# Kernel optimization log

Measured on AMD Instinct MI355X. Metric: run time of the kernel, lower is better.

## Reference

```python
import jax, jax.numpy as jnp
import numpy as np

N, E, R = 50000, 400000, 500
X_SIZE = 100
G_SIZE = 100
HID = 64
OUT = 64
HEADS = 2
ALPHA = 0.5
NEG_SLOPE = 0.01  # nn.LeakyReLU default and attention slope
EPS = 1e-12       # F.normalize eps


def _l2norm(x, axis):
    return x / jnp.maximum(jnp.linalg.norm(x, axis=axis, keepdims=True), EPS)


def _xavier(key, shape, gain=1.414):
    fan_in, fan_out = shape[-1], int(np.prod(shape[:-1]))
    std = gain * np.sqrt(2.0 / (fan_in + fan_out))
    return jax.random.normal(key, shape, dtype=jnp.float32) * std


def _att_layer(h, g, row, col, etype, W, b, att, out_size):
    # h: [N, D_h], g: [R, D_g], W: [heads*out, 2*D_h+D_g], att: [1, heads, out]
    n = h.shape[0]
    h_ijk = jnp.concatenate([h[row], h[col], g[etype]], axis=1)      # [E, 2D_h+D_g]
    c_ijk = (h_ijk @ W.T + b).reshape(-1, HEADS, out_size)           # [E, H, O]
    a = jnp.sum(att * c_ijk, axis=2, keepdims=True)                  # [E, H, 1]
    e = jnp.exp(jax.nn.leaky_relu(a, NEG_SLOPE))                     # unnormalized (matches torch exp w/o max-sub)
    denom = jax.ops.segment_sum(e, row, num_segments=n)              # [N, H, 1]
    alpha = e / denom[row]
    # self-edge zeros contribute nothing; segment_sum over num_segments=n is equivalent
    return jax.ops.segment_sum(alpha * c_ijk, col, num_segments=n)   # [N, H, O]


def setup_inputs() -> dict:
    key = jax.random.key(0)
    ks = jax.random.split(key, 20)
    x = jax.random.normal(ks[0], (N, X_SIZE), dtype=jnp.float32)
    g = jax.random.normal(ks[1], (R, G_SIZE), dtype=jnp.float32)
    edge_idx = jax.random.randint(ks[2], (2, E), 0, N)
    edge_type = jax.random.randint(ks[3], (E,), 0, R)
    d1 = 2 * X_SIZE + G_SIZE
    d2 = 2 * HID * HEADS + G_SIZE
    inp = {
        "x": x, "g": g, "edge_idx": edge_idx, "edge_type": edge_type,
        "W1i": _xavier(ks[4], (HEADS * HID, d1)), "b1i": jnp.zeros((HEADS * HID,), jnp.float32),
        "a1i": _xavier(ks[5], (1, HEADS, HID)),
        "W1o": _xavier(ks[6], (HEADS * HID, d1)), "b1o": jnp.zeros((HEADS * HID,), jnp.float32),
        "a1o": _xavier(ks[7], (1, HEADS, HID)),
        "W2i": _xavier(ks[8], (HEADS * OUT, d2)), "b2i": jnp.zeros((HEADS * OUT,), jnp.float32),
        "a2i": _xavier(ks[9], (1, HEADS, OUT)),
        "W2o": _xavier(ks[10], (HEADS * OUT, d2)), "b2o": jnp.zeros((HEADS * OUT,), jnp.float32),
        "a2o": _xavier(ks[11], (1, HEADS, OUT)),
        "We": _xavier(ks[12], (HID, X_SIZE)), "be": jnp.zeros((HID,), jnp.float32),
        "Wr": _xavier(ks[13], (HEADS * HID, G_SIZE)), "br": jnp.zeros((HEADS * HID,), jnp.float32),
    }
    return inp


def reference(x, g, edge_idx, edge_type, W1i, b1i, a1i, W1o, b1o, a1o,
              W2i, b2i, a2i, W2o, b2o, a2o, We, be, Wr, br):
    # x = F.normalize(x, dim=1).detach()
    xn = jax.lax.stop_gradient(_l2norm(x, axis=1))
    row, col = edge_idx[0], edge_idx[1]

    h_in = _att_layer(xn, g, row, col, edge_type, W1i, b1i, a1i, HID)
    h_out = _att_layer(xn, g, col, row, edge_type, W1o, b1o, a1o, HID)
    h = jax.nn.leaky_relu(ALPHA * h_in + (1.0 - ALPHA) * h_out, NEG_SLOPE)
    h = _l2norm(h, axis=2)                                # [N, H, HID]
    h = h.transpose(0, 1, 2).reshape(N, HEADS * HID)      # concat heads

    h_in = _att_layer(h, g, row, col, edge_type, W2i, b2i, a2i, OUT)
    h_out = _att_layer(h, g, col, row, edge_type, W2o, b2o, a2o, OUT)
    h = jax.nn.leaky_relu(ALPHA * h_in + (1.0 - ALPHA) * h_out, NEG_SLOPE)
    h = _l2norm(h, axis=2)                                # [N, H, OUT]

    # EntityLayer: Linear(x)[:, None, :] + h  (requires HID == OUT)
    h_prime = (xn @ We.T + be)[:, None, :] + h            # [N, H, OUT]
    h_prime = h_prime.reshape(N, HEADS * OUT)
    h_prime = _l2norm(h_prime, axis=1)                    # (torch dim=2 bug -> last dim)
    # _merge_heads stores mean but returns input unchanged

    g_prime = g @ Wr.T + br                               # [R, HEADS*HID]
    return h_prime, g_prime
```

## Files before the change

### kernel.cpp

```cpp
#include <hip/hip_runtime.h>

typedef unsigned short u16;
typedef unsigned int u32;
typedef short short8v __attribute__((ext_vector_type(8)));
typedef float float4v __attribute__((ext_vector_type(4)));

#define N_NODES 50000
#define E_EDGES 400000
#define R_REL   500
#define NKEYS   100000
#define SCAN_B  98
#define SEG     ((size_t)N_NODES * 128)

__device__ __forceinline__ float bl(u32 u){ return __uint_as_float(u << 16); }
__device__ __forceinline__ float bh(u32 u){ return __uint_as_float(u & 0xffff0000u); }
__device__ __forceinline__ u16 f2b(float f){
    u32 u = __float_as_uint(f);
    return (u16)((u + 0x7fffu + ((u >> 16) & 1u)) >> 16);
}
__device__ __forceinline__ u32 pk2(float a, float b){ return (u32)f2b(a) | ((u32)f2b(b) << 16); }
__device__ __forceinline__ float lrelu(float x){ return x > 0.f ? x : 0.01f * x; }

__global__ void k_norm_x(const float* __restrict__ x, u16* __restrict__ xnb){
    int wid = threadIdx.x >> 6, l = threadIdx.x & 63;
    int n = blockIdx.x * 4 + wid;
    if (n >= N_NODES) return;
    float v0 = x[(size_t)n * 100 + l];
    float v1 = (l + 64 < 100) ? x[(size_t)n * 100 + 64 + l] : 0.f;
    float ss = v0 * v0 + v1 * v1;
    #pragma unroll
    for (int m = 32; m; m >>= 1) ss += __shfl_xor(ss, m);
    float s = 1.f / fmaxf(sqrtf(ss), 1e-12f);
    xnb[(size_t)n * 128 + l] = f2b(v0 * s);
    xnb[(size_t)n * 128 + 64 + l] = (l + 64 < 100) ? f2b(v1 * s) : (u16)0;
}

__global__ void k_build_wcat(const float* __restrict__ W1i, const float* __restrict__ W1o,
                             const float* __restrict__ W2i, const float* __restrict__ W2o,
                             const float* __restrict__ We,
                             const float* __restrict__ a1i, const float* __restrict__ a1o,
                             const float* __restrict__ a2i, const float* __restrict__ a2o,
                             u16* __restrict__ wc1, u16* __restrict__ wc2,
                             float* __restrict__ attcat){
    int idx = blockIdx.x * blockDim.x + threadIdx.x;
    if (idx < 576 * 128){
        int r = idx >> 7, k = idx & 127;
        float v = 0.f;
        if (r < 512){
            int seg = r >> 7, rr = r & 127;
            const float* W = (seg < 2) ? W1i : W1o;
            int off = (seg & 1) ? 100 : 0;
            if (k < 100) v = W[(size_t)rr * 300 + off + k];
        } else {
            int rr = r - 512;
            if (k < 100) v = We[(size_t)rr * 100 + k];
        }
        wc1[idx] = f2b(v);
    } else if (idx < 576 * 128 + 512 * 128){
        int j = idx - 576 * 128;
        int r = j >> 7, k = j & 127;
        int seg = r >> 7, rr = r & 127;
        const float* W = (seg < 2) ? W2i : W2o;
        int off = (seg & 1) ? 128 : 0;
        wc2[j] = f2b(W[(size_t)rr * 356 + off + k]);
    } else if (idx < 576 * 128 + 512 * 128 + 1024){
        int j = idx - (576 * 128 + 512 * 128);
        int s = j >> 9, cc = j & 511;
        const float* a = s ? ((cc < 256) ? a2i : a2o) : ((cc < 256) ? a1i : a1o);
        attcat[j] = a[cc & 127];
    }
}

__global__ void k_pg(const float* __restrict__ g,
                     const float* __restrict__ W1i, const float* __restrict__ W1o,
                     const float* __restrict__ W2i, const float* __restrict__ W2o,
                     const float* __restrict__ b1i, const float* __restrict__ b1o,
                     const float* __restrict__ b2i, const float* __restrict__ b2o,
                     const float* __restrict__ a1i, const float* __restrict__ a1o,
                     const float* __restrict__ a2i, const float* __restrict__ a2o,
                     const float* __restrict__ Wr, const float* __restrict__ br,
                     float* __restrict__ Pg, float* __restrict__ qg,
                     float* __restrict__ out){
    int bid = blockIdx.x;
    int j = threadIdx.x;
    __shared__ float gs[100];
    __shared__ float red[128];
    if (bid >= 2000){
        int r = bid - 2000;
        if (j < 100) gs[j] = g[(size_t)r * 100 + j];
        __syncthreads();
        float acc = br[j];
        #pragma unroll 4
        for (int k = 0; k < 100; ++k) acc += gs[k] * Wr[(size_t)j * 100 + k];
        out[(size_t)N_NODES * 128 + (size_t)r * 128 + j] = acc;
        return;
    }
    int r = bid >> 2, t = bid & 3;
    const float *W, *b, *att; int ld, off;
    if (t == 0){ W = W1i; ld = 300; off = 200; b = b1i; att = a1i; }
    else if (t == 1){ W = W1o; ld = 300; off = 200; b = b1o; att = a1o; }
    else if (t == 2){ W = W2i; ld = 356; off = 256; b = b2i; att = a2i; }
    else { W = W2o; ld = 356; off = 256; b = b2o; att = a2o; }
    if (j < 100) gs[j] = g[(size_t)r * 100 + j];
    __syncthreads();
    float acc = b[j];
    #pragma unroll 4
    for (int k = 0; k < 100; ++k) acc += gs[k] * W[(size_t)j * ld + off + k];
    Pg[((size_t)t * R_REL + r) * 128 + j] = acc;
    red[j] = att[j] * acc;
    __syncthreads();
    if (j < 2){
        float s = 0.f;
        for (int k = 0; k < 64; ++k) s += red[j * 64 + k];
        qg[((size_t)t * R_REL + r) * 2 + j] = s;
    }
}

__launch_bounds__(256)
__global__ void k_gemm(const u16* __restrict__ A, const u16* __restrict__ W,
                       const float* __restrict__ attcat,
                       u16* __restrict__ NPt, float* __restrict__ q, int M, int NN){
    __shared__ __align__(16) char lds[4 * 16 * 272];
    int l = threadIdx.x & 63, w = threadIdx.x >> 6;
    int rb = blockIdx.x * 64 + w * 16;
    int grp = blockIdx.y;
    int cb = grp * 128;
    int ncols = NN - cb; if (ncols > 128) ncols = 128;
    int tiles = ncols >> 4;
    int rowW = (ncols == 128) ? 128 : 64;
    int pitch = rowW * 2 + 16;
    char* lw = lds + w * 16 * pitch;

    int ar = rb + (l & 15); if (ar >= M) ar = M - 1;
    const u16* Ap = A + (size_t)ar * 128 + (l >> 4) * 8;
    short8v a0 = *(const short8v*)(Ap);
    short8v a1 = *(const short8v*)(Ap + 32);
    short8v a2 = *(const short8v*)(Ap + 64);
    short8v a3 = *(const short8v*)(Ap + 96);
    float qa[4] = {0.f, 0.f, 0.f, 0.f};
    bool doq = (cb < 512);
    int rloc0 = (l >> 4) * 4;
    for (int t = 0; t < tiles; ++t){
        int cc = cb + t * 16 + (l & 15);
        const u16* Wp = W + (size_t)cc * 128 + (l >> 4) * 8;
        short8v b0 = *(const short8v*)(Wp);
        short8v b1 = *(const short8v*)(Wp + 32);
        short8v b2 = *(const short8v*)(Wp + 64);
        short8v b3 = *(const short8v*)(Wp + 96);
        float4v acc = {0.f, 0.f, 0.f, 0.f};
        acc = __builtin_amdgcn_mfma_f32_16x16x32_bf16(a0, b0, acc, 0, 0, 0);
        acc = __builtin_amdgcn_mfma_f32_16x16x32_bf16(a1, b1, acc, 0, 0, 0);
        acc = __builtin_amdgcn_mfma_f32_16x16x32_bf16(a2, b2, acc, 0, 0, 0);
        acc = __builtin_amdgcn_mfma_f32_16x16x32_bf16(a3, b3, acc, 0, 0, 0);
        int lcol = t * 16 + (l & 15);
        #pragma unroll
        for (int r = 0; r < 4; ++r)
            *(u16*)(lw + (size_t)(rloc0 + r) * pitch + lcol * 2) = f2b(acc[r]);
        if (doq){
            float av = attcat[cc];
            #pragma unroll
            for (int r = 0; r < 4; ++r) qa[r] += av * acc[r];
            if ((t & 3) == 3){
                int g = (cb >> 6) + (t >> 2);
                #pragma unroll
                for (int r = 0; r < 4; ++r){
                    float s = qa[r];
                    s += __shfl_xor(s, 1); s += __shfl_xor(s, 2);
                    s += __shfl_xor(s, 4); s += __shfl_xor(s, 8);
                    if ((l & 15) == 0){
                        int rr = rb + rloc0 + r;
                        if (rr < M) q[(size_t)rr * 8 + g] = s;
                    }
                    qa[r] = 0.f;
                }
            }
        }
    }
    __syncthreads();
    u16* gb = (rowW == 128) ? (NPt + (size_t)grp * SEG + (size_t)rb * 128)
                            : (NPt + 4 * SEG + (size_t)rb * 64);
    int chunks = (rowW == 128) ? 4 : 2;
    for (int i = 0; i < chunks; ++i){
        int u = i * 512 + l * 8;
        int rloc = (rowW == 128) ? (u >> 7) : (u >> 6);
        int c    = (rowW == 128) ? (u & 127) : (u & 63);
        if (rb + rloc < M){
            short8v v = *(const short8v*)(lw + (size_t)rloc * pitch + c * 2);
            *(short8v*)(gb + u) = v;
        }
    }
}

__global__ void k_hist(const int* __restrict__ ei, u32* __restrict__ cnt){
    int e = blockIdx.x * blockDim.x + threadIdx.x;
    if (e >= E_EDGES) return;
    atomicAdd(&cnt[ei[E_EDGES + e]], 1u);
    atomicAdd(&cnt[N_NODES + ei[e]], 1u);
}

__launch_bounds__(1024)
__global__ void k_scan1(const u32* __restrict__ cnt, u32* __restrict__ off, u32* __restrict__ bsum){
    __shared__ u32 sh[1024];
    int t = threadIdx.x, b = blockIdx.x, idx = b * 1024 + t;
    u32 v = cnt[idx];
    sh[t] = v; __syncthreads();
    #pragma unroll
    for (int d = 1; d < 1024; d <<= 1){
        u32 add = (t >= d) ? sh[t - d] : 0;
        __syncthreads();
        sh[t] += add;
        __syncthreads();
    }
    off[idx] = sh[t] - v;
    if (t == 1023) bsum[b] = sh[1023];
}

__launch_bounds__(1024)
__global__ void k_scan3(u32* __restrict__ off, const u32* __restrict__ bsum,
                        u32* __restrict__ cur){
    __shared__ u32 baseb;
    if (threadIdx.x == 0){
        u32 run = 0;
        for (int i = 0; i < (int)blockIdx.x; ++i) run += bsum[i];
        baseb = run;
    }
    __syncthreads();
    int idx = blockIdx.x * 1024 + threadIdx.x;
    u32 v = off[idx] + baseb;
    off[idx] = v;
    if (idx < NKEYS) cur[idx] = v;
}

__global__ void k_pos(const int* __restrict__ ei, const int* __restrict__ ety,
                      u32* __restrict__ cur,
                      u32* __restrict__ Pso, u32* __restrict__ Pss){
    int e = blockIdx.x * blockDim.x + threadIdx.x;
    if (e >= E_EDGES) return;
    u32 row = (u32)ei[e], col = (u32)ei[E_EDGES + e];
    u32 etb = (u32)ety[e] << 20;
    u32 pI = atomicAdd(&cur[col], 1u);
    Pso[pI] = row | etb;  Pss[pI] = col;
    u32 pO = atomicAdd(&cur[N_NODES + row], 1u);
    Pso[pO] = col | etb;  Pss[pO] = row;
}

__global__ void k_edgeA(const u32* __restrict__ Pso, const u32* __restrict__ Pss,
                        const float* __restrict__ q,
                        const float* __restrict__ qgI, const float* __restrict__ qgO,
                        float2* __restrict__ ex){
    int p = blockIdx.x * blockDim.x + threadIdx.x;
    if (p >= 2 * E_EDGES) return;
    u32 so = Pso[p], self = Pss[p];
    u32 oth = so & 0xFFFFF, et = so >> 20;
    float2 r;
    if (p < E_EDGES){
        r.x = expf(lrelu(q[(size_t)oth * 8 + 0] + q[(size_t)self * 8 + 2] + qgI[(size_t)et * 2 + 0]));
        r.y = expf(lrelu(q[(size_t)oth * 8 + 1] + q[(size_t)self * 8 + 3] + qgI[(size_t)et * 2 + 1]));
    } else {
        r.x = expf(lrelu(q[(size_t)oth * 8 + 4] + q[(size_t)self * 8 + 6] + qgO[(size_t)et * 2 + 0]));
        r.y = expf(lrelu(q[(size_t)oth * 8 + 5] + q[(size_t)self * 8 + 7] + qgO[(size_t)et * 2 + 1]));
    }
    ex[p] = r;
}

__global__ void k_denom(const u32* __restrict__ off, const u32* __restrict__ Pso,
                        const float* __restrict__ q,
                        const float* __restrict__ qgI, const float* __restrict__ qgO,
                        float* __restrict__ rdI, float* __restrict__ rdO){
    int t = blockIdx.x * blockDim.x + threadIdx.x;
    if (t >= 2 * N_NODES) return;
    if (t < N_NODES){
        int n = t;
        float qn0 = q[(size_t)n * 8 + 0], qn1 = q[(size_t)n * 8 + 1];
        float s0 = 0.f, s1 = 0.f;
        for (u32 p = off[N_NODES + n]; p < off[N_NODES + n + 1]; ++p){
            u32 so = Pso[p]; u32 oth = so & 0xFFFFFu, et = so >> 20;
            float2 qo = *(const float2*)(q + (size_t)oth * 8 + 2);
            float2 gq = *(const float2*)(qgI + (size_t)et * 2);
            s0 += expf(lrelu(qn0 + qo.x + gq.x));
            s1 += expf(lrelu(qn1 + qo.y + gq.y));
        }
        rdI[(size_t)n * 2 + 0] = (s0 > 0.f) ? 1.f / s0 : 0.f;
        rdI[(size_t)n * 2 + 1] = (s1 > 0.f) ? 1.f / s1 : 0.f;
    } else {
        int n = t - N_NODES;
        float qn4 = q[(size_t)n * 8 + 4], qn5 = q[(size_t)n * 8 + 5];
        float s0 = 0.f, s1 = 0.f;
        for (u32 p = off[n]; p < off[n + 1]; ++p){
            u32 so = Pso[p]; u32 oth = so & 0xFFFFFu, et = so >> 20;
            float2 qo = *(const float2*)(q + (size_t)oth * 8 + 6);
            float2 gq = *(const float2*)(qgO + (size_t)et * 2);
            s0 += expf(lrelu(qn4 + qo.x + gq.x));
            s1 += expf(lrelu(qn5 + qo.y + gq.y));
        }
        rdO[(size_t)n * 2 + 0] = (s0 > 0.f) ? 1.f / s0 : 0.f;
        rdO[(size_t)n * 2 + 1] = (s1 > 0.f) ? 1.f / s1 : 0.f;
    }
}

__launch_bounds__(256)
__global__ void k_agg(const u32* __restrict__ off,
                      const u32* __restrict__ Pso,
                      const float2* __restrict__ ex,
                      const u16* __restrict__ NPt,
                      const float* __restrict__ PgI, const float* __restrict__ PgO,
                      const float* __restrict__ rdI, const float* __restrict__ rdO,
                      int final_stage,
                      const u16* __restrict__ NPt1, const float* __restrict__ be,
                      u16* __restrict__ h1b, float* __restrict__ out){
    int wid = threadIdx.x >> 6, l = threadIdx.x & 63;
    int n = blockIdx.x * 4 + wid;
    if (n >= N_NODES) return;
    int h = l >> 5, d0 = l * 2;
    const u16* PaI = NPt;
    const u16* PbI = NPt + SEG;
    const u16* PaO = NPt + 2 * SEG;
    const u16* PbO = NPt + 3 * SEG;
    u32 pbi = *(const u32*)(PbI + (size_t)n * 128 + d0);
    u32 pbo = *(const u32*)(PbO + (size_t)n * 128 + d0);

    float a0 = 0.f, a1 = 0.f, sai = 0.f;
    {
        u32 sBeg = __builtin_amdgcn_readfirstlane(off[n]);
        u32 sEnd = __builtin_amdgcn_readfirstlane(off[n + 1]);
        for (u32 p = sBeg; p < sEnd; p += 8){
            u32 so[8]; float2 e2[8];
            #pragma unroll
            for (int j = 0; j < 8; ++j){
                u32 idx = p + j; if (idx >= sEnd) idx = sEnd - 1;
                so[j] = Pso[idx];
                e2[j] = ex[idx];
            }
            float w0[8], w1[8]; u32 pa[8]; float2 gv[8];
            #pragma unroll
            for (int j = 0; j < 8; ++j){
                u32 oth = so[j] & 0xFFFFFu, et = so[j] >> 20;
                float2 rd2 = *(const float2*)(rdI + (size_t)oth * 2);
                float sc = (p + j < sEnd) ? 1.f : 0.f;
                w0[j] = e2[j].x * rd2.x * sc;
                w1[j] = e2[j].y * rd2.y * sc;
                pa[j] = *(const u32*)(PaI + (size_t)oth * 128 + d0);
                gv[j] = *(const float2*)(PgI + (size_t)et * 128 + d0);
            }
            #pragma unroll
            for (int j = 0; j < 8; ++j){
                float w = h ? w1[j] : w0[j];
                a0 += w * (bl(pa[j]) + gv[j].x);
                a1 += w * (bh(pa[j]) + gv[j].y);
                sai += w;
            }
        }
    }
    a0 += sai * bl(pbi);
    a1 += sai * bh(pbi);

    float b0 = 0.f, b1 = 0.f, sao = 0.f;
    {
        u32 sBeg = __builtin_amdgcn_readfirstlane(off[N_NODES + n]);
        u32 sEnd = __builtin_amdgcn_readfirstlane(off[N_NODES + n + 1]);
        for (u32 p = sBeg; p < sEnd; p += 8){
            u32 so[8]; float2 e2[8];
            #pragma unroll
            for (int j = 0; j < 8; ++j){
                u32 idx = p + j; if (idx >= sEnd) idx = sEnd - 1;
                so[j] = Pso[idx];
                e2[j] = ex[idx];
            }
            float w0[8], w1[8]; u32 pa[8]; float2 gv[8];
            #pragma unroll
            for (int j = 0; j < 8; ++j){
                u32 oth = so[j] & 0xFFFFFu, et = so[j] >> 20;
                float2 rd2 = *(const float2*)(rdO + (size_t)oth * 2);
                float sc = (p + j < sEnd) ? 1.f : 0.f;
                w0[j] = e2[j].x * rd2.x * sc;
                w1[j] = e2[j].y * rd2.y * sc;
                pa[j] = *(const u32*)(PaO + (size_t)oth * 128 + d0);
                gv[j] = *(const float2*)(PgO + (size_t)et * 128 + d0);
            }
            #pragma unroll
            for (int j = 0; j < 8; ++j){
                float w = h ? w1[j] : w0[j];
                b0 += w * (bl(pa[j]) + gv[j].x);
                b1 += w * (bh(pa[j]) + gv[j].y);
                sao += w;
            }
        }
    }
    b0 += sao * bl(pbo);
    b1 += sao * bh(pbo);

    float vx = lrelu(0.5f * (a0 + b0));
    float vy = lrelu(0.5f * (a1 + b1));
    float ss = vx * vx + vy * vy;
    #pragma unroll
    for (int m = 16; m; m >>= 1) ss += __shfl_xor(ss, m);
    float s2 = 1.f / fmaxf(sqrtf(ss), 1e-12f);
    if (!final_stage){
        *(u32*)(h1b + (size_t)n * 128 + d0) = pk2(vx * s2, vy * s2);
    } else {
        float h20 = vx * s2, h21 = vy * s2;
        int o0 = d0 & 63;
        u32 ue = *(const u32*)(NPt1 + 4 * SEG + (size_t)n * 64 + o0);
        float hp0 = bl(ue) + be[o0] + h20;
        float hp1 = bh(ue) + be[o0 + 1] + h21;
        float st = hp0 * hp0 + hp1 * hp1;
        #pragma unroll
        for (int m = 32; m; m >>= 1) st += __shfl_xor(st, m);
        float s = 1.f / fmaxf(sqrtf(st), 1e-12f);
        float2 o; o.x = hp0 * s; o.y = hp1 * s;
        *(float2*)(out + (size_t)n * 128 + d0) = o;
    }
}

extern "C" void kernel_launch(void* const* d_in, const int* in_sizes, int n_in,
                              void* d_out, int out_size, void* d_ws, size_t ws_size,
                              hipStream_t stream){
    const float* x   = (const float*)d_in[0];
    const float* g   = (const float*)d_in[1];
    const int*   ei  = (const int*)d_in[2];
    const int*   ety = (const int*)d_in[3];
    const float* W1i = (const float*)d_in[4];
    const float* b1i = (const float*)d_in[5];
    const float* a1i = (const float*)d_in[6];
    const float* W1o = (const float*)d_in[7];
    const float* b1o = (const float*)d_in[8];
    const float* a1o = (const float*)d_in[9];
    const float* W2i = (const float*)d_in[10];
    const float* b2i = (const float*)d_in[11];
    const float* a2i = (const float*)d_in[12];
    const float* W2o = (const float*)d_in[13];
    const float* b2o = (const float*)d_in[14];
    const float* a2o = (const float*)d_in[15];
    const float* We  = (const float*)d_in[16];
    const float* be  = (const float*)d_in[17];
    const float* Wr  = (const float*)d_in[18];
    const float* br  = (const float*)d_in[19];
    float* out = (float*)d_out;

    char* ws = (char*)d_ws;
    size_t off_b = 0;
    auto carve = [&](size_t bytes) -> char* {
        char* p = ws + off_b;
        off_b += (bytes + 255) & ~(size_t)255;
        return p;
    };
    u16*    xnb   = (u16*)carve((size_t)N_NODES * 128 * 2);
    u16*    wc1   = (u16*)carve((size_t)576 * 128 * 2);
    u16*    wc2   = (u16*)carve((size_t)512 * 128 * 2);
    float*  attct = (float*)carve((size_t)1024 * 4);
    u16*    NPt1  = (u16*)carve((SEG * 4 + (size_t)N_NODES * 64) * 2);
    u16*    NPt2  = (u16*)carve(SEG * 4 * 2);
    u16*    h1b   = (u16*)carve((size_t)N_NODES * 128 * 2);
    float*  q     = (float*)carve((size_t)N_NODES * 8 * 4);
    float*  Pg    = (float*)carve((size_t)4 * R_REL * 128 * 4);
    float*  qg    = (float*)carve((size_t)4 * R_REL * 2 * 4);
    u32*    cnt   = (u32*)carve((size_t)SCAN_B * 1024 * 4);
    u32*    offA  = (u32*)carve((size_t)SCAN_B * 1024 * 4);
    u32*    cur   = (u32*)carve((size_t)NKEYS * 4);
    u32*    bsum  = (u32*)carve((size_t)SCAN_B * 4);
    u32*    Pso   = (u32*)carve((size_t)2 * E_EDGES * 4);
    u32*    Pss   = (u32*)carve((size_t)2 * E_EDGES * 4);
    float2* ex    = (float2*)carve((size_t)2 * E_EDGES * 8);
    float*  rdI   = (float*)carve((size_t)N_NODES * 2 * 4);
    float*  rdO   = (float*)carve((size_t)N_NODES * 2 * 4);

    hipMemsetAsync(cnt, 0, (size_t)SCAN_B * 1024 * 4, stream);
    k_hist<<<1563, 256, 0, stream>>>(ei, cnt);
    k_scan1<<<SCAN_B, 1024, 0, stream>>>(cnt, offA, bsum);
    k_scan3<<<SCAN_B, 1024, 0, stream>>>(offA, bsum, cur);
    k_pos<<<1563, 256, 0, stream>>>(ei, ety, cur, Pso, Pss);

    k_norm_x<<<12500, 256, 0, stream>>>(x, xnb);
    k_build_wcat<<<548, 256, 0, stream>>>(W1i, W1o, W2i, W2o, We,
                                          a1i, a1o, a2i, a2o, wc1, wc2, attct);
    k_pg<<<2500, 128, 0, stream>>>(g, W1i, W1o, W2i, W2o, b1i, b1o, b2i, b2o,
                                   a1i, a1o, a2i, a2o, Wr, br, Pg, qg, out);

    k_gemm<<<dim3(782, 5), 256, 0, stream>>>(xnb, wc1, attct, NPt1, q, N_NODES, 576);
    k_edgeA<<<3125, 256, 0, stream>>>(Pso, Pss, q, qg, qg + R_REL * 2, ex);
    k_denom<<<391, 256, 0, stream>>>(offA, Pso, q, qg, qg + R_REL * 2, rdI, rdO);
    k_agg<<<12500, 256, 0, stream>>>(offA, Pso, ex, NPt1, Pg, Pg + R_REL * 128,
                                     rdI, rdO, 0, NPt1, be, h1b, out);

    k_gemm<<<dim3(782, 4), 256, 0, stream>>>(h1b, wc2, attct + 512, NPt2, q, N_NODES, 512);
    k_edgeA<<<3125, 256, 0, stream>>>(Pso, Pss, q, qg + 2 * R_REL * 2, qg + 3 * R_REL * 2, ex);
    k_denom<<<391, 256, 0, stream>>>(offA, Pso, q, qg + 2 * R_REL * 2, qg + 3 * R_REL * 2,
                                     rdI, rdO);
    k_agg<<<12500, 256, 0, stream>>>(offA, Pso, ex, NPt2, Pg + 2 * R_REL * 128,
                                     Pg + 3 * R_REL * 128, rdI, rdO, 1, NPt1, be, h1b, out);
}
```

Measured before the change: 432.6 us.

## Split aggregation wave into two half-waves processing alternate edges with 4-wide loads

Rewrites the aggregation kernel so each half of the 64-lane wave handles alternate edges. Each lane covers 4 feature elements using 8-byte bf16 and 16-byte float loads, and the two halves are combined with a cross-half shuffle at the end. The in and out directions are merged into one unrolled loop, and each iteration covers 16 edges instead of 8. This aims to raise memory-level parallelism and use wider gathers in a latency-bound sparse gather, at the cost of extra shuffles, more registers and half the lanes sitting idle on the final store.

```diff
diff --git a/kernel.cpp b/kernel.cpp
--- a/kernel.cpp
+++ b/kernel.cpp
@@ -311,104 +311,89 @@
     int wid = threadIdx.x >> 6, l = threadIdx.x & 63;
     int n = blockIdx.x * 4 + wid;
     if (n >= N_NODES) return;
-    int h = l >> 5, d0 = l * 2;
-    const u16* PaI = NPt;
-    const u16* PbI = NPt + SEG;
-    const u16* PaO = NPt + 2 * SEG;
-    const u16* PbO = NPt + 3 * SEG;
-    u32 pbi = *(const u32*)(PbI + (size_t)n * 128 + d0);
-    u32 pbo = *(const u32*)(PbO + (size_t)n * 128 + d0);
-
-    float a0 = 0.f, a1 = 0.f, sai = 0.f;
-    {
-        u32 sBeg = __builtin_amdgcn_readfirstlane(off[n]);
-        u32 sEnd = __builtin_amdgcn_readfirstlane(off[n + 1]);
-        for (u32 p = sBeg; p < sEnd; p += 8){
+    int half = l >> 5, hl = l & 31;
+    int d0 = hl * 4;
+    int headLane = hl >> 4;
+    float acc0 = 0.f, acc1 = 0.f, acc2 = 0.f, acc3 = 0.f;
+
+    #pragma unroll
+    for (int dir = 0; dir < 2; ++dir){
+        const u16* Pa  = NPt + (dir ? 2 * SEG : 0);
+        const u16* Pb  = NPt + (dir ? 3 * SEG : SEG);
+        const float* Pgd = dir ? PgO : PgI;
+        const float* rd  = dir ? rdO : rdI;
+        int key = dir ? (N_NODES + n) : n;
+        u32 sBeg = off[key], sEnd = off[key + 1];
+        float sw = 0.f;
+        for (u32 p = sBeg; p < sEnd; p += 16){
             u32 so[8]; float2 e2[8];
             #pragma unroll
             for (int j = 0; j < 8; ++j){
-                u32 idx = p + j; if (idx >= sEnd) idx = sEnd - 1;
+                u32 idx = p + 2 * j + half;
+                if (idx >= sEnd) idx = sEnd - 1;
                 so[j] = Pso[idx];
                 e2[j] = ex[idx];
             }
-            float w0[8], w1[8]; u32 pa[8]; float2 gv[8];
+            float w[8]; uint2 pa[8]; float4 gv[8];
             #pragma unroll
             for (int j = 0; j < 8; ++j){
                 u32 oth = so[j] & 0xFFFFFu, et = so[j] >> 20;
-                float2 rd2 = *(const float2*)(rdI + (size_t)oth * 2);
-                float sc = (p + j < sEnd) ? 1.f : 0.f;
-                w0[j] = e2[j].x * rd2.x * sc;
-                w1[j] = e2[j].y * rd2.y * sc;
-                pa[j] = *(const u32*)(PaI + (size_t)oth * 128 + d0);
-                gv[j] = *(const float2*)(PgI + (size_t)et * 128 + d0);
+                float2 rd2 = *(const float2*)(rd + (size_t)oth * 2);
+                float sc = (p + 2 * j + half < sEnd) ? 1.f : 0.f;
+                float w0 = e2[j].x * rd2.x, w1 = e2[j].y * rd2.y;
+                w[j] = (headLane ? w1 : w0) * sc;
+                pa[j] = *(const uint2*)(Pa + (size_t)oth * 128 + d0);
+                gv[j] = *(const float4*)(Pgd + (size_t)et * 128 + d0);
             }
             #pragma unroll
             for (int j = 0; j < 8; ++j){
-                float w = h ? w1[j] : w0[j];
-                a0 += w * (bl(pa[j]) + gv[j].x);
-                a1 += w * (bh(pa[j]) + gv[j].y);
-                sai += w;
+                acc0 += w[j] * (bl(pa[j].x) + gv[j].x);
+                acc1 += w[j] * (bh(pa[j].x) + gv[j].y);
+                acc2 += w[j] * (bl(pa[j].y) + gv[j].z);
+                acc3 += w[j] * (bh(pa[j].y) + gv[j].w);
+                sw += w[j];
             }
         }
-    }
-    a0 += sai * bl(pbi);
-    a1 += sai * bh(pbi);
-
-    float b0 = 0.f, b1 = 0.f, sao = 0.f;
-    {
-        u32 sBeg = __builtin_amdgcn_readfirstlane(off[N_NODES + n]);
-        u32 sEnd = __builtin_amdgcn_readfirstlane(off[N_NODES + n + 1]);
-        for (u32 p = sBeg; p < sEnd; p += 8){
-            u32 so[8]; float2 e2[8];
-            #pragma unroll
-            for (int j = 0; j < 8; ++j){
-                u32 idx = p + j; if (idx >= sEnd) idx = sEnd - 1;
-                so[j] = Pso[idx];
-                e2[j] = ex[idx];
-            }
-            float w0[8], w1[8]; u32 pa[8]; float2 gv[8];
-            #pragma unroll
-            for (int j = 0; j < 8; ++j){
-                u32 oth = so[j] & 0xFFFFFu, et = so[j] >> 20;
-                float2 rd2 = *(const float2*)(rdO + (size_t)oth * 2);
-                float sc = (p + j < sEnd) ? 1.f : 0.f;
-                w0[j] = e2[j].x * rd2.x * sc;
-                w1[j] = e2[j].y * rd2.y * sc;
-                pa[j] = *(const u32*)(PaO + (size_t)oth * 128 + d0);
-                gv[j] = *(const float2*)(PgO + (size_t)et * 128 + d0);
-            }
-            #pragma unroll
-            for (int j = 0; j < 8; ++j){
-                float w = h ? w1[j] : w0[j];
-                b0 += w * (bl(pa[j]) + gv[j].x);
-                b1 += w * (bh(pa[j]) + gv[j].y);
-                sao += w;
-            }
-        }
-    }
-    b0 += sao * bl(pbo);
-    b1 += sao * bh(pbo);
-
-    float vx = lrelu(0.5f * (a0 + b0));
-    float vy = lrelu(0.5f * (a1 + b1));
-    float ss = vx * vx + vy * vy;
+        uint2 pb = *(const uint2*)(Pb + (size_t)n * 128 + d0);
+        acc0 += sw * bl(pb.x);
+        acc1 += sw * bh(pb.x);
+        acc2 += sw * bl(pb.y);
+        acc3 += sw * bh(pb.y);
+    }
+
+    acc0 += __shfl_xor(acc0, 32);
+    acc1 += __shfl_xor(acc1, 32);
+    acc2 += __shfl_xor(acc2, 32);
+    acc3 += __shfl_xor(acc3, 32);
+
+    float v0 = lrelu(0.5f * acc0), v1 = lrelu(0.5f * acc1);
+    float v2 = lrelu(0.5f * acc2), v3 = lrelu(0.5f * acc3);
+    float ssl = v0 * v0 + v1 * v1 + v2 * v2 + v3 * v3;
     #pragma unroll
-    for (int m = 16; m; m >>= 1) ss += __shfl_xor(ss, m);
-    float s2 = 1.f / fmaxf(sqrtf(ss), 1e-12f);
+    for (int m = 8; m; m >>= 1) ssl += __shfl_xor(ssl, m);
+    float s2 = 1.f / fmaxf(sqrtf(ssl), 1e-12f);
     if (!final_stage){
-        *(u32*)(h1b + (size_t)n * 128 + d0) = pk2(vx * s2, vy * s2);
+        if (half == 0){
+            uint2 o; o.x = pk2(v0 * s2, v1 * s2); o.y = pk2(v2 * s2, v3 * s2);
+            *(uint2*)(h1b + (size_t)n * 128 + d0) = o;
+        }
     } else {
-        float h20 = vx * s2, h21 = vy * s2;
+        float h20 = v0 * s2, h21 = v1 * s2, h22 = v2 * s2, h23 = v3 * s2;
         int o0 = d0 & 63;
-        u32 ue = *(const u32*)(NPt1 + 4 * SEG + (size_t)n * 64 + o0);
-        float hp0 = bl(ue) + be[o0] + h20;
-        float hp1 = bh(ue) + be[o0 + 1] + h21;
-        float st = hp0 * hp0 + hp1 * hp1;
+        uint2 ue = *(const uint2*)(NPt1 + 4 * SEG + (size_t)n * 64 + o0);
+        float4 bev = *(const float4*)(be + o0);
+        float hp0 = bl(ue.x) + bev.x + h20;
+        float hp1 = bh(ue.x) + bev.y + h21;
+        float hp2 = bl(ue.y) + bev.z + h22;
+        float hp3 = bh(ue.y) + bev.w + h23;
+        float st = hp0 * hp0 + hp1 * hp1 + hp2 * hp2 + hp3 * hp3;
         #pragma unroll
-        for (int m = 32; m; m >>= 1) st += __shfl_xor(st, m);
+        for (int m = 16; m; m >>= 1) st += __shfl_xor(st, m);
         float s = 1.f / fmaxf(sqrtf(st), 1e-12f);
-        float2 o; o.x = hp0 * s; o.y = hp1 * s;
-        *(float2*)(out + (size_t)n * 128 + d0) = o;
+        if (half == 0){
+            float4 o; o.x = hp0 * s; o.y = hp1 * s; o.z = hp2 * s; o.w = hp3 * s;
+            *(float4*)(out + (size_t)n * 128 + d0) = o;
+        }
     }
 }
 
```

After: 514.1 us. +18.8%, slower.
